# Performance work log

Measured on AMD Instinct MI355X. Metric: run time of the kernel, lower is better.

Reference implementation:

```python
import jax, jax.numpy as jnp
import numpy as np


def conv2d(x, w, b=None, pad=0):
    # x: [B,C,H,W], w: [O,I,kh,kw]
    out = jax.lax.conv_general_dilated(
        x, w, window_strides=(1, 1), padding=[(pad, pad), (pad, pad)],
        dimension_numbers=('NCHW', 'OIHW', 'NCHW'))
    if b is not None:
        out = out + b[None, :, None, None]
    return out


def setup_inputs() -> dict:
    key = jax.random.key(0)
    ks = jax.random.split(key, 10)
    B, C, W, H, N, G = 8, 256, 64, 64, 1024, 32
    s = jnp.float32(0.02)  # small init so softmax is not saturated
    return {
        'input_graph': jax.random.normal(ks[0], (B, N, G), jnp.float32),
        'input_image': jax.random.normal(ks[1], (B, C, W, H), jnp.float32),
        'Wq': jax.random.normal(ks[2], (C, C), jnp.float32) * s,
        'bq': jnp.zeros((C,), jnp.float32),
        'Wk': jax.random.normal(ks[3], (C, G), jnp.float32) * s,
        'bk': jnp.zeros((C,), jnp.float32),
        'Wv': jax.random.normal(ks[4], (C, G), jnp.float32) * s,
        'bv': jnp.zeros((C,), jnp.float32),
        'conv1_w': jax.random.normal(ks[5], (C, C, 1, 1), jnp.float32) * s,
        'bn_gamma': jnp.ones((C,), jnp.float32),
        'bn_beta': jnp.zeros((C,), jnp.float32),
        'bn_mean': jnp.zeros((C,), jnp.float32),
        'bn_var': jnp.ones((C,), jnp.float32),
        'conv2_w': jax.random.normal(ks[6], (C, C, 3, 3), jnp.float32) * s,
        'conv2_b': jnp.zeros((C,), jnp.float32),
        'conv3_w': jax.random.normal(ks[7], (C, C, 1, 1), jnp.float32) * s,
        'conv3_b': jnp.zeros((C,), jnp.float32),
    }


def reference(input_graph, input_image, Wq, bq, Wk, bk, Wv, bv,
              conv1_w, bn_gamma, bn_beta, bn_mean, bn_var,
              conv2_w, conv2_b, conv3_w, conv3_b):
    B, C, W, H = input_image.shape
    P = W * H
    g = jnp.transpose(input_graph, (0, 2, 1))  # [B,G,N]
    # 1x1 conv1d projections == per-position matmuls
    K = jnp.einsum('og,bgn->bon', Wk, g) + bk[None, :, None]   # [B,C,N]
    V = jnp.einsum('og,bgn->bon', Wv, g) + bv[None, :, None]   # [B,C,N]
    x = input_image.reshape(B, C, P)
    Q = jnp.einsum('oc,bcp->bop', Wq, x) + bq[None, :, None]   # [B,C,P]
    # att[b,p,n] = sum_c Q[b,c,p] * K[b,c,n]  (Q was permuted to [B,P,C] in torch)
    att = jnp.einsum('bcp,bcn->bpn', Q, K) / jnp.sqrt(jnp.float32(C))
    # NOTE: original applies Softmax(dim=1) -> over the P (pixel) axis
    att = jax.nn.softmax(att, axis=1)
    # message = V @ att^T : [B,C,N] x [B,N,P] -> [B,C,P]
    msg = jnp.einsum('bcn,bpn->bcp', V, att).reshape(B, C, W, H)
    # Conv_Bn_Activation: 1x1 conv (no bias) + BN (inference) + LeakyReLU(0.1)
    h = conv2d(msg, conv1_w)
    inv = jax.lax.rsqrt(bn_var + jnp.float32(1e-5))
    h = (h - bn_mean[None, :, None, None]) * (bn_gamma * inv)[None, :, None, None] + bn_beta[None, :, None, None]
    h = jnp.where(h > 0, h, jnp.float32(0.1) * h)
    h = conv2d(h, conv2_w, conv2_b, pad=1)  # 3x3, pad 1
    return input_image + conv2d(h, conv3_w, conv3_b)  # 1x1
```

## Files before the change

### kernel.cpp

```cpp
#include <hip/hip_runtime.h>
#include <hip/hip_bf16.h>

typedef __hip_bfloat16 bf16;
typedef unsigned short u16;
typedef __attribute__((ext_vector_type(8))) short  b8v;
typedef __attribute__((ext_vector_type(8))) unsigned short u16x8;
typedef __attribute__((ext_vector_type(4))) unsigned short u16x4;
typedef __attribute__((ext_vector_type(4))) float f32x4;

static __device__ __forceinline__ float us2f(u16 s) {
    unsigned int u = ((unsigned int)s) << 16;
    return __builtin_bit_cast(float, u);
}
static __device__ __forceinline__ u16 f2us(float x) {
    union { bf16 h; u16 s; } v; v.h = __float2bfloat16(x); return v.s;
}
static __device__ __forceinline__ float b2f(bf16 x) { return __bfloat162float(x); }
static __device__ __forceinline__ bf16 f2b(float x) { return __float2bfloat16(x); }
static __device__ __forceinline__ float toF(float x) { return x; }
static __device__ __forceinline__ float toF(bf16 x)  { return b2f(x); }
static __device__ __forceinline__ void stor(float* p, float v) { *p = v; }
static __device__ __forceinline__ void stor(bf16* p,  float v) { *p = f2b(v); }

static __device__ __forceinline__ void gload16(const u16* g, u16* l) {
    __builtin_amdgcn_global_load_lds(
        (const __attribute__((address_space(1))) unsigned int*)g,
        (__attribute__((address_space(3))) unsigned int*)l,
        16, 0, 0);
}


__global__ __launch_bounds__(256) void cast_f2b4(const float* __restrict__ src,
                                                 u16* __restrict__ dst, int n4)
{
    int i = blockIdx.x * 256 + threadIdx.x;
    if (i < n4) {
        float4 v = ((const float4*)src)[i];
        u16x4 o = { f2us(v.x), f2us(v.y), f2us(v.z), f2us(v.w) };
        ((u16x4*)dst)[i] = o;
    }
}

__global__ __launch_bounds__(256) void repack_w2(const float* __restrict__ src,
                                                 u16* __restrict__ dst)
{
    int idx = blockIdx.x * 256 + threadIdx.x;
    int o = idx / 2304, k = idx - o * 2304;
    int tap = k >> 8, c = k & 255;
    dst[idx] = f2us(src[(o * 256 + c) * 9 + tap]);
}

__global__ __launch_bounds__(256) void transpose_cast_x(const float* __restrict__ x,
                                                        u16* __restrict__ xT, int C, int P)
{
    __shared__ u16 t[64][72];
    const int b = blockIdx.z, c0 = blockIdx.y * 64, p0 = blockIdx.x * 64;
    const int tid = threadIdx.x;
    const int r = tid >> 2, q = tid & 3;
    const float* src = x + ((size_t)b * C + c0 + r) * P + p0 + q * 16;
#pragma unroll
    for (int i = 0; i < 16; i++) t[q * 16 + i][r] = f2us(src[i]);
    __syncthreads();
    u16* dst = xT + ((size_t)b * P + p0 + r) * C + c0 + q * 16;
    *(u16x8*)dst       = *(u16x8*)&t[r][q * 16];
    *(u16x8*)(dst + 8) = *(u16x8*)&t[r][q * 16 + 8];
}

template<int EPI, typename TA, typename TB, typename TC>
__global__ __launch_bounds__(256) void gemm_any(
    const TA* __restrict__ A, const TB* __restrict__ B, TC* __restrict__ C,
    int M, int Nn, int Kd,
    long saM, long saK, long aB,
    long sbK, long sbN, long bB,
    long scM, long scN, long cB,
    float scale, const float* __restrict__ bias)
{
    __shared__ float As[16][65];
    __shared__ float Bs[16][65];
    const int b  = blockIdx.z;
    const TA* Ab = A + (long)b * aB;
    const TB* Bb = B + (long)b * bB;
    const int m0 = blockIdx.y * 64, n0 = blockIdx.x * 64;
    const int tid = threadIdx.x;
    const int tx = tid & 15, ty = tid >> 4;
    const bool kfA = (saK == 1);
    const bool nfB = (sbN == 1);
    float acc[4][4] = {};

    for (int k0 = 0; k0 < Kd; k0 += 16) {
#pragma unroll
        for (int i = 0; i < 4; i++) {
            int idx = tid + i * 256; int mm, kk;
            if (kfA) { kk = idx & 15; mm = idx >> 4; }
            else     { mm = idx & 63; kk = idx >> 6; }
            As[kk][mm] = toF(Ab[(long)(m0 + mm) * saM + (long)(k0 + kk) * saK]);
        }
#pragma unroll
        for (int i = 0; i < 4; i++) {
            int idx = tid + i * 256; int nn, kk;
            if (nfB) { nn = idx & 63; kk = idx >> 6; }
            else     { kk = idx & 15; nn = idx >> 4; }
            Bs[kk][nn] = toF(Bb[(long)(k0 + kk) * sbK + (long)(n0 + nn) * sbN]);
        }
        __syncthreads();
#pragma unroll
        for (int kk = 0; kk < 16; kk++) {
            float a[4], bb[4];
#pragma unroll
            for (int i = 0; i < 4; i++) a[i]  = As[kk][ty * 4 + i];
#pragma unroll
            for (int j = 0; j < 4; j++) bb[j] = Bs[kk][tx * 4 + j];
#pragma unroll
            for (int i = 0; i < 4; i++)
#pragma unroll
                for (int j = 0; j < 4; j++) acc[i][j] += a[i] * bb[j];
        }
        __syncthreads();
    }
#pragma unroll
    for (int i = 0; i < 4; i++) {
        int m = m0 + ty * 4 + i;
        float add0 = (EPI == 0 && bias) ? bias[m] : 0.f;
#pragma unroll
        for (int j = 0; j < 4; j++) {
            int n = n0 + tx * 4 + j;
            float v = acc[i][j] * scale + add0;
            if (EPI == 3 && bias) v += bias[n];
            stor(&C[(long)b * cB + (long)m * scM + (long)n * scN], v);
        }
    }
}

template<int EPI, bool CT, typename TC, int NTILE>
__global__ __launch_bounds__(256) void gemm_mfma(
    const u16* __restrict__ A, const u16* __restrict__ Bt, TC* __restrict__ Cc,
    int M, int N, int K, int lda, int ldb, int ldc,
    long aBat, long bBat, long cBat,
    float scale, const float* __restrict__ bias,
    const float* __restrict__ gamma, const float* __restrict__ beta,
    const float* __restrict__ mean,  const float* __restrict__ var,
    const float* __restrict__ resid, long rBat, int ldr)
{
    constexpr int NI = NTILE / 32;
    __shared__ u16 Al[128 * 32];
    __shared__ u16 Bl[NTILE * 32];
    const int bat = blockIdx.z;
    const int m0 = blockIdx.y * 128, n0 = blockIdx.x * NTILE;
    const int tid = threadIdx.x;
    const int lane = tid & 63, wid = tid >> 6;
    const int wr = wid >> 1, wc = wid & 1;
    const int fr = lane & 15, fq = lane >> 4;

    const u16* gA = A  + (size_t)bat * aBat + (size_t)(m0 + wid * 32 + (lane >> 2)) * lda + (lane & 3) * 8;
    const u16* gB = Bt + (size_t)bat * bBat + (size_t)(n0 + wid * (NTILE / 4) + (lane >> 2)) * ldb + (lane & 3) * 8;
    u16* lA = &Al[(wid * 32) * 32];
    u16* lB = &Bl[(wid * (NTILE / 4)) * 32];
    const size_t a16 = (size_t)16 * lda, b16 = (size_t)16 * ldb;

    f32x4 acc[4][NI];
#pragma unroll
    for (int i = 0; i < 4; i++)
#pragma unroll
        for (int j = 0; j < NI; j++) acc[i][j] = (f32x4){0.f, 0.f, 0.f, 0.f};

    for (int k0 = 0; k0 < K; k0 += 32) {
        gload16(gA + k0,       lA);
        gload16(gA + k0 + a16, lA + 16 * 32);
        gload16(gB + k0,       lB);
        if constexpr (NTILE == 128) gload16(gB + k0 + b16, lB + 16 * 32);
        __syncthreads();
        b8v a[4], b[NI];
#pragma unroll
        for (int mi = 0; mi < 4; mi++) a[mi] = *(const b8v*)&Al[(wr * 64 + mi * 16 + fr) * 32 + fq * 8];
#pragma unroll
        for (int ni = 0; ni < NI; ni++) b[ni] = *(const b8v*)&Bl[(wc * (NTILE / 2) + ni * 16 + fr) * 32 + fq * 8];
#pragma unroll
        for (int mi = 0; mi < 4; mi++)
#pragma unroll
            for (int ni = 0; ni < NI; ni++)
                acc[mi][ni] = __builtin_amdgcn_mfma_f32_16x16x32_bf16(a[mi], b[ni], acc[mi][ni], 0, 0, 0);
        __syncthreads();
    }

    const int mbase = m0 + wr * 64, nbase = n0 + wc * (NTILE / 2);
#pragma unroll
    for (int mi = 0; mi < 4; mi++) {
        float esc[4], ead[4];
#pragma unroll
        for (int j = 0; j < 4; j++) {
            int m = mbase + mi * 16 + fq * 4 + j;
            if (EPI == 1) {
                float sc = gamma[m] * rsqrtf(var[m] + 1e-5f);
                esc[j] = sc; ead[j] = beta[m] - mean[m] * sc;
            } else {
                esc[j] = scale; ead[j] = (EPI != 3 && bias) ? bias[m] : 0.f;
            }
        }
#pragma unroll
        for (int ni = 0; ni < NI; ni++) {
            f32x4 v = acc[mi][ni];
            const int n = nbase + ni * 16 + fr;
            if (CT) {
                const int mb = mbase + mi * 16 + fq * 4;
                u16x4 pk;
#pragma unroll
                for (int j = 0; j < 4; j++) {
                    float x = v[j] * esc[j] + ead[j];
                    if (EPI == 1) x = x > 0.f ? x : 0.1f * x;
                    pk[j] = f2us(x);
                }
                *(u16x4*)((u16*)Cc + (size_t)bat * cBat + (size_t)n * ldc + mb) = pk;
            } else {
#pragma unroll
                for (int j = 0; j < 4; j++) {
                    int m = mbase + mi * 16 + fq * 4 + j;
                    float x;
                    if (EPI == 3) x = __expf(v[j] * esc[j]);
                    else {
                        x = v[j] * esc[j] + ead[j];
                        if (EPI == 1) x = x > 0.f ? x : 0.1f * x;
                        if (EPI == 2) x += resid[(size_t)bat * rBat + (size_t)m * ldr + n];
                    }
                    TC* p = Cc + (size_t)bat * cBat + (size_t)m * ldc + n;
                    if constexpr (sizeof(TC) == 2) *(u16*)p = f2us(x); else *(float*)p = x;
                }
            }
        }
    }
}

__global__ __launch_bounds__(256) void conv3x3_mfma(
    const u16* __restrict__ Wt, const u16* __restrict__ X, u16* __restrict__ Y,
    const float* __restrict__ bias)
{
    const int C = 256, P = 4096, K = 2304;
    __shared__ u16 Al[2][128 * 32];
    __shared__ u16 Bl[2][64 * 32];
    const int bat = blockIdx.z;
    const int m0 = blockIdx.y * 128, n0 = blockIdx.x * 64;
    const int y0 = blockIdx.x;
    const int tid = threadIdx.x;
    const int lane = tid & 63, wid = tid >> 6;
    const int wr = wid >> 1, wc = wid & 1;
    const int fr = lane & 15, fq = lane >> 4;
    const int bx = tid & 63, cg = tid >> 6;

    const u16* Ag = Wt + (size_t)(m0 + wid * 32 + (lane >> 2)) * K + (lane & 3) * 8;
    u16* lA0 = &Al[0][(wid * 32) * 32];
    u16* lA1 = &Al[1][(wid * 32) * 32];
    const u16* Xb = X + (size_t)bat * C * P;

    f32x4 acc[4][2];
#pragma unroll
    for (int i = 0; i < 4; i++)
#pragma unroll
        for (int j = 0; j < 2; j++) acc[i][j] = (f32x4){0.f, 0.f, 0.f, 0.f};

    u16x8 breg[2];
    auto loadB = [&](int k0) {
        const int tap = k0 >> 8;
        const int c0k = (k0 & 255) + cg * 16;
        const int dy = tap / 3 - 1, dxv = tap - (tap / 3) * 3 - 1;
        const int y = y0 + dy, xs = bx + dxv;
        const bool ok = ((unsigned)y < 64u) && ((unsigned)xs < 64u);
        const int off = ok ? (y * 64 + xs) : 0;
#pragma unroll
        for (int g = 0; g < 2; g++) {
            const u16* src = Xb + (size_t)(c0k + g * 8) * P + off;
            u16x8 v;
#pragma unroll
            for (int l = 0; l < 8; l++) v[l] = src[(size_t)l * P];
            if (!ok) v = (u16x8){0, 0, 0, 0, 0, 0, 0, 0};
            breg[g] = v;
        }
    };

    loadB(0);

    for (int k0 = 0; k0 < K; k0 += 64) {
        gload16(Ag + k0,                       lA0);
        gload16(Ag + k0 + (size_t)16 * K,      lA0 + 16 * 32);
        gload16(Ag + k0 + 32,                  lA1);
        gload16(Ag + k0 + 32 + (size_t)16 * K, lA1 + 16 * 32);
        *(u16x8*)&Bl[cg >> 1][bx * 32 + (cg & 1) * 16]     = breg[0];
        *(u16x8*)&Bl[cg >> 1][bx * 32 + (cg & 1) * 16 + 8] = breg[1];
        __syncthreads();
        if (k0 + 64 < K) loadB(k0 + 64);
#pragma unroll
        for (int t = 0; t < 2; t++) {
            b8v a[4], b[2];
#pragma unroll
            for (int mi = 0; mi < 4; mi++) a[mi] = *(const b8v*)&Al[t][(wr * 64 + mi * 16 + fr) * 32 + fq * 8];
#pragma unroll
            for (int ni = 0; ni < 2; ni++) b[ni] = *(const b8v*)&Bl[t][(wc * 32 + ni * 16 + fr) * 32 + fq * 8];
#pragma unroll
            for (int mi = 0; mi < 4; mi++)
#pragma unroll
                for (int ni = 0; ni < 2; ni++)
                    acc[mi][ni] = __builtin_amdgcn_mfma_f32_16x16x32_bf16(a[mi], b[ni], acc[mi][ni], 0, 0, 0);
        }
        __syncthreads();
    }

    const int mbase = m0 + wr * 64, nbase = n0 + wc * 32;
#pragma unroll
    for (int mi = 0; mi < 4; mi++) {
        const int mb = mbase + mi * 16 + fq * 4;
        float bb[4];
#pragma unroll
        for (int j = 0; j < 4; j++) bb[j] = bias[mb + j];
#pragma unroll
        for (int ni = 0; ni < 2; ni++) {
            const int n = nbase + ni * 16 + fr;
            u16x4 pk;
#pragma unroll
            for (int j = 0; j < 4; j++) pk[j] = f2us(acc[mi][ni][j] + bb[j]);
            *(u16x4*)&Y[(size_t)bat * P * C + (size_t)n * C + mb] = pk;
        }
    }
}

__global__ __launch_bounds__(256) void colsum_partial(const u16* __restrict__ E,
                                                      float* __restrict__ part,
                                                      int P, int N, int PC)
{
    const int b = blockIdx.z, chunk = blockIdx.y, n = blockIdx.x * 64 + (threadIdx.x & 63);
    const int pg = threadIdx.x >> 6;
    const int csz = P / PC, p0 = chunk * csz;
    const u16* col = E + ((size_t)b * P + p0) * N + n;
    float s = 0.f;
    for (int i = pg; i < csz; i += 4) s += us2f(col[(size_t)i * N]);
    __shared__ float ss[4][64];
    ss[pg][threadIdx.x & 63] = s;
    __syncthreads();
    if (pg == 0) {
        const int nl = threadIdx.x & 63;
        part[((size_t)b * PC + chunk) * N + n] = ss[0][nl] + ss[1][nl] + ss[2][nl] + ss[3][nl];
    }
}

__global__ __launch_bounds__(256) void colsum_merge(const float* __restrict__ part,
                                                    float* __restrict__ sinv, int N, int PC)
{
    const int n = blockIdx.x * 256 + threadIdx.x, b = blockIdx.y;
    const float* pc = part + (size_t)b * PC * N + n;
    float s = 0.f;
    for (int c = 0; c < PC; c++) s += pc[(size_t)c * N];
    sinv[(size_t)b * N + n] = 1.f / s;
}

__global__ __launch_bounds__(256) void scale_v(u16* __restrict__ V,
                                               const float* __restrict__ sinv,
                                               int C, int N)
{
    const size_t base = ((size_t)blockIdx.x * 256 + threadIdx.x) * 8;
    const int n0 = (int)(base % N);
    const int b = (int)(base / ((size_t)C * N));
    const float* sv = sinv + (size_t)b * N + n0;
    u16x8 v = *(u16x8*)&V[base];
#pragma unroll
    for (int j = 0; j < 8; j++) v[j] = f2us(us2f(v[j]) * sv[j]);
    *(u16x8*)&V[base] = v;
}


extern "C" void kernel_launch(void* const* d_in, const int* in_sizes, int n_in,
                              void* d_out, int out_size, void* d_ws, size_t ws_size,
                              hipStream_t stream)
{
    const float* graph = (const float*)d_in[0];
    const float* image = (const float*)d_in[1];
    const float* Wq  = (const float*)d_in[2];
    const float* bq  = (const float*)d_in[3];
    const float* Wk  = (const float*)d_in[4];
    const float* bk  = (const float*)d_in[5];
    const float* Wv  = (const float*)d_in[6];
    const float* bv  = (const float*)d_in[7];
    const float* c1w = (const float*)d_in[8];
    const float* gam = (const float*)d_in[9];
    const float* bet = (const float*)d_in[10];
    const float* mea = (const float*)d_in[11];
    const float* var = (const float*)d_in[12];
    const float* c2w = (const float*)d_in[13];
    const float* c2b = (const float*)d_in[14];
    const float* c3w = (const float*)d_in[15];
    const float* c3b = (const float*)d_in[16];
    float* out = (float*)d_out;

    const int B = 8, C = 256, P = 4096, N = 1024, G = 32;
    const int PC = 16;
    const size_t MiB = 1024 * 1024, KiB = 1024;
    char* ws = (char*)d_ws;
    u16* E     = (u16*)(ws);
    u16* xT    = (u16*)(ws);
    u16* Wq_b  = (u16*)(ws + 16 * MiB);
    u16* Qt    = (u16*)(ws + 64 * MiB);
    u16* msgT  = Qt;
    float* sinv = (float*)(ws + 80 * MiB);
    u16* c1w_b = (u16*)(ws + 80 * MiB + 64 * KiB);
    u16* c3w_b = (u16*)(ws + 80 * MiB + 192 * KiB);
    u16* c2w_b = (u16*)(ws + 80 * MiB + 320 * KiB);
    float* part = (float*)(ws + 82 * MiB);
    u16* Kt    = (u16*)(ws + 80 * MiB);
    u16* Vb    = (u16*)(ws + 84 * MiB);
    u16* h1    = (u16*)(ws);
    u16* h2T   = (u16*)(ws + 16 * MiB);

    transpose_cast_x<<<dim3(P / 64, C / 64, B), 256, 0, stream>>>(image, xT, C, P);
    cast_f2b4<<<64,  256, 0, stream>>>(Wq,  Wq_b,  16384);
    gemm_any<3, float, float, bf16><<<dim3(C / 64, N / 64, B), 256, 0, stream>>>(
        graph, Wk, (bf16*)Kt, N, C, G,
        G, 1, (long)N * G,   1, G, 0,   C, 1, (long)N * C, 1.f, bk);
    gemm_any<0, float, float, bf16><<<dim3(N / 64, C / 64, B), 256, 0, stream>>>(
        Wv, graph, (bf16*)Vb, C, N, G,
        G, 1, 0,   1, G, (long)N * G,   N, 1, (long)C * N, 1.f, bv);

    gemm_mfma<0, true, u16, 64><<<dim3(P / 64, C / 128, B), 256, 0, stream>>>(
        Wq_b, xT, Qt, C, P, C, C, C, C,
        0, (long)P * C, (long)P * C, 1.f, bq,
        nullptr, nullptr, nullptr, nullptr, nullptr, 0, 0);
    gemm_mfma<3, false, u16, 128><<<dim3(N / 128, P / 128, B), 256, 0, stream>>>(
        Qt, Kt, E, P, N, C, C, C, N,
        (long)P * C, (long)N * C, (long)P * N, 0.0625f, nullptr,
        nullptr, nullptr, nullptr, nullptr, nullptr, 0, 0);
    cast_f2b4<<<64,   256, 0, stream>>>(c1w, c1w_b, 16384);
    cast_f2b4<<<64,   256, 0, stream>>>(c3w, c3w_b, 16384);
    repack_w2<<<2304, 256, 0, stream>>>(c2w, c2w_b);
    colsum_partial<<<dim3(N / 64, PC, B), 256, 0, stream>>>(E, part, P, N, PC);
    colsum_merge<<<dim3(N / 256, B), 256, 0, stream>>>(part, sinv, N, PC);
    scale_v<<<dim3((int)((size_t)B * C * N / 8 / 256)), 256, 0, stream>>>(Vb, sinv, C, N);
    gemm_mfma<0, true, u16, 64><<<dim3(P / 64, C / 128, B), 256, 0, stream>>>(
        Vb, E, msgT, C, P, N, N, N, C,
        (long)C * N, (long)P * N, (long)P * C, 1.f, nullptr,
        nullptr, nullptr, nullptr, nullptr, nullptr, 0, 0);
    gemm_mfma<1, false, u16, 64><<<dim3(P / 64, C / 128, B), 256, 0, stream>>>(
        c1w_b, msgT, h1, C, P, C, C, C, P,
        0, (long)P * C, (long)C * P, 1.f, nullptr,
        gam, bet, mea, var, nullptr, 0, 0);
    conv3x3_mfma<<<dim3(P / 64, C / 128, B), 256, 0, stream>>>(c2w_b, h1, h2T, c2b);
    gemm_mfma<2, false, float, 64><<<dim3(P / 64, C / 128, B), 256, 0, stream>>>(
        c3w_b, h2T, out, C, P, C, C, C, P,
        0, (long)P * C, (long)C * P, 1.f, c3b,
        nullptr, nullptr, nullptr, nullptr, image, (long)C * P, P);
}
```

Measured before the change: 256.4 us.

## Fuse softmax column sums into attention GEMM epilogue and swizzle LDS layouts

The exp-attention GEMM now accumulates per-column partial sums in its epilogue, reduces them with wave shuffles and shared memory, and writes per-row-block partials. This removes the separate colsum_partial kernel that re-read the whole E matrix. Separately, the LDS tiles in the MFMA GEMM and the 3x3 conv use an XOR swizzle on the k-chunk index to reduce bank conflicts on the fragment reads. The partial buffer now reuses the output buffer as scratch, and the merge step reduces over more partials (P/128 instead of 16).

```diff
diff --git a/kernel.cpp b/kernel.cpp
--- a/kernel.cpp
+++ b/kernel.cpp
@@ -139,20 +139,24 @@
     float scale, const float* __restrict__ bias,
     const float* __restrict__ gamma, const float* __restrict__ beta,
     const float* __restrict__ mean,  const float* __restrict__ var,
-    const float* __restrict__ resid, long rBat, int ldr)
+    const float* __restrict__ resid, long rBat, int ldr,
+    float* __restrict__ csum)
 {
     constexpr int NI = NTILE / 32;
     __shared__ u16 Al[128 * 32];
     __shared__ u16 Bl[NTILE * 32];
+    __shared__ float red[2][2][4][16];
     const int bat = blockIdx.z;
     const int m0 = blockIdx.y * 128, n0 = blockIdx.x * NTILE;
     const int tid = threadIdx.x;
     const int lane = tid & 63, wid = tid >> 6;
     const int wr = wid >> 1, wc = wid & 1;
     const int fr = lane & 15, fq = lane >> 4;
-
-    const u16* gA = A  + (size_t)bat * aBat + (size_t)(m0 + wid * 32 + (lane >> 2)) * lda + (lane & 3) * 8;
-    const u16* gB = Bt + (size_t)bat * bBat + (size_t)(n0 + wid * (NTILE / 4) + (lane >> 2)) * ldb + (lane & 3) * 8;
+    const int sc = ((lane & 3) ^ ((lane >> 3) & 3)) * 8;
+    const int axs = (fq ^ ((fr >> 1) & 3)) * 8;
+
+    const u16* gA = A  + (size_t)bat * aBat + (size_t)(m0 + wid * 32 + (lane >> 2)) * lda + sc;
+    const u16* gB = Bt + (size_t)bat * bBat + (size_t)(n0 + wid * (NTILE / 4) + (lane >> 2)) * ldb + sc;
     u16* lA = &Al[(wid * 32) * 32];
     u16* lB = &Bl[(wid * (NTILE / 4)) * 32];
     const size_t a16 = (size_t)16 * lda, b16 = (size_t)16 * ldb;
@@ -171,9 +175,9 @@
         __syncthreads();
         b8v a[4], b[NI];
 #pragma unroll
-        for (int mi = 0; mi < 4; mi++) a[mi] = *(const b8v*)&Al[(wr * 64 + mi * 16 + fr) * 32 + fq * 8];
-#pragma unroll
-        for (int ni = 0; ni < NI; ni++) b[ni] = *(const b8v*)&Bl[(wc * (NTILE / 2) + ni * 16 + fr) * 32 + fq * 8];
+        for (int mi = 0; mi < 4; mi++) a[mi] = *(const b8v*)&Al[(wr * 64 + mi * 16 + fr) * 32 + axs];
+#pragma unroll
+        for (int ni = 0; ni < NI; ni++) b[ni] = *(const b8v*)&Bl[(wc * (NTILE / 2) + ni * 16 + fr) * 32 + axs];
 #pragma unroll
         for (int mi = 0; mi < 4; mi++)
 #pragma unroll
@@ -183,6 +187,9 @@
     }
 
     const int mbase = m0 + wr * 64, nbase = n0 + wc * (NTILE / 2);
+    float cs[NI];
+#pragma unroll
+    for (int ni = 0; ni < NI; ni++) cs[ni] = 0.f;
 #pragma unroll
     for (int mi = 0; mi < 4; mi++) {
         float esc[4], ead[4];
@@ -190,8 +197,8 @@
         for (int j = 0; j < 4; j++) {
             int m = mbase + mi * 16 + fq * 4 + j;
             if (EPI == 1) {
-                float sc = gamma[m] * rsqrtf(var[m] + 1e-5f);
-                esc[j] = sc; ead[j] = beta[m] - mean[m] * sc;
+                float sc2 = gamma[m] * rsqrtf(var[m] + 1e-5f);
+                esc[j] = sc2; ead[j] = beta[m] - mean[m] * sc2;
             } else {
                 esc[j] = scale; ead[j] = (EPI != 3 && bias) ? bias[m] : 0.f;
             }
@@ -215,7 +222,7 @@
                 for (int j = 0; j < 4; j++) {
                     int m = mbase + mi * 16 + fq * 4 + j;
                     float x;
-                    if (EPI == 3) x = __expf(v[j] * esc[j]);
+                    if (EPI == 3) { x = __expf(v[j] * esc[j]); cs[ni] += x; }
                     else {
                         x = v[j] * esc[j] + ead[j];
                         if (EPI == 1) x = x > 0.f ? x : 0.1f * x;
@@ -225,6 +232,21 @@
                     if constexpr (sizeof(TC) == 2) *(u16*)p = f2us(x); else *(float*)p = x;
                 }
             }
+        }
+    }
+    if constexpr (EPI == 3) {
+#pragma unroll
+        for (int ni = 0; ni < NI; ni++) {
+            float s = cs[ni];
+            s += __shfl_xor(s, 16, 64);
+            s += __shfl_xor(s, 32, 64);
+            if (fq == 0) red[wr][wc][ni][fr] = s;
+        }
+        __syncthreads();
+        if (tid < NTILE) {
+            const int wcc = tid >> 6, nii = (tid >> 4) & 3, frr = tid & 15;
+            float s = red[0][wcc][nii][frr] + red[1][wcc][nii][frr];
+            csum[((size_t)bat * gridDim.y + blockIdx.y) * ldc + n0 + tid] = s;
         }
     }
 }
@@ -244,8 +266,12 @@
     const int wr = wid >> 1, wc = wid & 1;
     const int fr = lane & 15, fq = lane >> 4;
     const int bx = tid & 63, cg = tid >> 6;
-
-    const u16* Ag = Wt + (size_t)(m0 + wid * 32 + (lane >> 2)) * K + (lane & 3) * 8;
+    const int scA = ((lane & 3) ^ ((lane >> 3) & 3)) * 8;
+    const int axs = (fq ^ ((fr >> 1) & 3)) * 8;
+    const int bf = (bx >> 1) & 3;
+    const int bc0 = (cg & 1) * 2;
+
+    const u16* Ag = Wt + (size_t)(m0 + wid * 32 + (lane >> 2)) * K + scA;
     u16* lA0 = &Al[0][(wid * 32) * 32];
     u16* lA1 = &Al[1][(wid * 32) * 32];
     const u16* Xb = X + (size_t)bat * C * P;
@@ -282,17 +308,17 @@
         gload16(Ag + k0 + (size_t)16 * K,      lA0 + 16 * 32);
         gload16(Ag + k0 + 32,                  lA1);
         gload16(Ag + k0 + 32 + (size_t)16 * K, lA1 + 16 * 32);
-        *(u16x8*)&Bl[cg >> 1][bx * 32 + (cg & 1) * 16]     = breg[0];
-        *(u16x8*)&Bl[cg >> 1][bx * 32 + (cg & 1) * 16 + 8] = breg[1];
+        *(u16x8*)&Bl[cg >> 1][bx * 32 + (bc0 ^ bf) * 8]       = breg[0];
+        *(u16x8*)&Bl[cg >> 1][bx * 32 + ((bc0 + 1) ^ bf) * 8] = breg[1];
         __syncthreads();
         if (k0 + 64 < K) loadB(k0 + 64);
 #pragma unroll
         for (int t = 0; t < 2; t++) {
             b8v a[4], b[2];
 #pragma unroll
-            for (int mi = 0; mi < 4; mi++) a[mi] = *(const b8v*)&Al[t][(wr * 64 + mi * 16 + fr) * 32 + fq * 8];
-#pragma unroll
-            for (int ni = 0; ni < 2; ni++) b[ni] = *(const b8v*)&Bl[t][(wc * 32 + ni * 16 + fr) * 32 + fq * 8];
+            for (int mi = 0; mi < 4; mi++) a[mi] = *(const b8v*)&Al[t][(wr * 64 + mi * 16 + fr) * 32 + axs];
+#pragma unroll
+            for (int ni = 0; ni < 2; ni++) b[ni] = *(const b8v*)&Bl[t][(wc * 32 + ni * 16 + fr) * 32 + axs];
 #pragma unroll
             for (int mi = 0; mi < 4; mi++)
 #pragma unroll
@@ -317,25 +343,6 @@
             for (int j = 0; j < 4; j++) pk[j] = f2us(acc[mi][ni][j] + bb[j]);
             *(u16x4*)&Y[(size_t)bat * P * C + (size_t)n * C + mb] = pk;
         }
-    }
-}
-
-__global__ __launch_bounds__(256) void colsum_partial(const u16* __restrict__ E,
-                                                      float* __restrict__ part,
-                                                      int P, int N, int PC)
-{
-    const int b = blockIdx.z, chunk = blockIdx.y, n = blockIdx.x * 64 + (threadIdx.x & 63);
-    const int pg = threadIdx.x >> 6;
-    const int csz = P / PC, p0 = chunk * csz;
-    const u16* col = E + ((size_t)b * P + p0) * N + n;
-    float s = 0.f;
-    for (int i = pg; i < csz; i += 4) s += us2f(col[(size_t)i * N]);
-    __shared__ float ss[4][64];
-    ss[pg][threadIdx.x & 63] = s;
-    __syncthreads();
-    if (pg == 0) {
-        const int nl = threadIdx.x & 63;
-        part[((size_t)b * PC + chunk) * N + n] = ss[0][nl] + ss[1][nl] + ss[2][nl] + ss[3][nl];
     }
 }
 
@@ -388,7 +395,6 @@
     float* out = (float*)d_out;
 
     const int B = 8, C = 256, P = 4096, N = 1024, G = 32;
-    const int PC = 16;
     const size_t MiB = 1024 * 1024, KiB = 1024;
     char* ws = (char*)d_ws;
     u16* E     = (u16*)(ws);
@@ -400,11 +406,11 @@
     u16* c1w_b = (u16*)(ws + 80 * MiB + 64 * KiB);
     u16* c3w_b = (u16*)(ws + 80 * MiB + 192 * KiB);
     u16* c2w_b = (u16*)(ws + 80 * MiB + 320 * KiB);
-    float* part = (float*)(ws + 82 * MiB);
     u16* Kt    = (u16*)(ws + 80 * MiB);
     u16* Vb    = (u16*)(ws + 84 * MiB);
     u16* h1    = (u16*)(ws);
     u16* h2T   = (u16*)(ws + 16 * MiB);
+    float* part = out;
 
     transpose_cast_x<<<dim3(P / 64, C / 64, B), 256, 0, stream>>>(image, xT, C, P);
     cast_f2b4<<<64,  256, 0, stream>>>(Wq,  Wq_b,  16384);
@@ -418,28 +424,27 @@
     gemm_mfma<0, true, u16, 64><<<dim3(P / 64, C / 128, B), 256, 0, stream>>>(
         Wq_b, xT, Qt, C, P, C, C, C, C,
         0, (long)P * C, (long)P * C, 1.f, bq,
-        nullptr, nullptr, nullptr, nullptr, nullptr, 0, 0);
+        nullptr, nullptr, nullptr, nullptr, nullptr, 0, 0, nullptr);
     gemm_mfma<3, false, u16, 128><<<dim3(N / 128, P / 128, B), 256, 0, stream>>>(
         Qt, Kt, E, P, N, C, C, C, N,
         (long)P * C, (long)N * C, (long)P * N, 0.0625f, nullptr,
-        nullptr, nullptr, nullptr, nullptr, nullptr, 0, 0);
+        nullptr, nullptr, nullptr, nullptr, nullptr, 0, 0, part);
     cast_f2b4<<<64,   256, 0, stream>>>(c1w, c1w_b, 16384);
     cast_f2b4<<<64,   256, 0, stream>>>(c3w, c3w_b, 16384);
     repack_w2<<<2304, 256, 0, stream>>>(c2w, c2w_b);
-    colsum_partial<<<dim3(N / 64, PC, B), 256, 0, stream>>>(E, part, P, N, PC);
-    colsum_merge<<<dim3(N / 256, B), 256, 0, stream>>>(part, sinv, N, PC);
+    colsum_merge<<<dim3(N / 256, B), 256, 0, stream>>>(part, sinv, N, P / 128);
     scale_v<<<dim3((int)((size_t)B * C * N / 8 / 256)), 256, 0, stream>>>(Vb, sinv, C, N);
     gemm_mfma<0, true, u16, 64><<<dim3(P / 64, C / 128, B), 256, 0, stream>>>(
         Vb, E, msgT, C, P, N, N, N, C,
         (long)C * N, (long)P * N, (long)P * C, 1.f, nullptr,
-        nullptr, nullptr, nullptr, nullptr, nullptr, 0, 0);
+        nullptr, nullptr, nullptr, nullptr, nullptr, 0, 0, nullptr);
     gemm_mfma<1, false, u16, 64><<<dim3(P / 64, C / 128, B), 256, 0, stream>>>(
         c1w_b, msgT, h1, C, P, C, C, C, P,
         0, (long)P * C, (long)C * P, 1.f, nullptr,
-        gam, bet, mea, var, nullptr, 0, 0);
+        gam, bet, mea, var, nullptr, 0, 0, nullptr);
     conv3x3_mfma<<<dim3(P / 64, C / 128, B), 256, 0, stream>>>(c2w_b, h1, h2T, c2b);
     gemm_mfma<2, false, float, 64><<<dim3(P / 64, C / 128, B), 256, 0, stream>>>(
         c3w_b, h2T, out, C, P, C, C, C, P,
         0, (long)P * C, (long)C * P, 1.f, c3b,
-        nullptr, nullptr, nullptr, nullptr, image, (long)C * P, P);
-}
+        nullptr, nullptr, nullptr, nullptr, image, (long)C * P, P, nullptr);
+}
```

Result: faster. 231.2 us (-9.8%).
